# Optimization experiments

Measured on AMD Instinct MI355X. Metric: run time of the kernel, lower is better.

The kernel has to match this reference:

```python
import jax, jax.numpy as jnp
import numpy as np

B = 4096

def conv2d(x, w, b):
    # x: [B,C,H,W], w: [O,I,kh,kw]
    y = jax.lax.conv_general_dilated(x, w, (1, 1), 'VALID',
                                     dimension_numbers=('NCHW', 'OIHW', 'NCHW'))
    return y + b[None, :, None, None]

def maxpool2(x):
    return jax.lax.reduce_window(x, -jnp.inf, jax.lax.max,
                                 (1, 1, 2, 2), (1, 1, 2, 2), 'VALID')

def mdlstm(x, Wx, Whl, Whu, b, H, W, hid):
    # x: [B, C_in, H*W]; 2D LSTM scan over the HxW grid.
    Bn = x.shape[0]
    # Precompute input contribution for all cells: [H, W, B, 5*hid]
    xg = (jnp.einsum('bcn,gc->nbg', x, Wx) + b).reshape(H, W, Bn, 5 * hid)

    def row_step(carry, xg_row):
        h_up_row, c_up_row = carry  # [W, B, hid] from previous row

        def col_step(cc, inp):
            h_left, c_left = cc
            g_ij, h_up, c_up = inp
            g = g_ij + h_left @ Whl.T + h_up @ Whu.T
            i, f1, f2, o, gg = jnp.split(g, 5, axis=-1)
            c = (jax.nn.sigmoid(f1) * c_left + jax.nn.sigmoid(f2) * c_up
                 + jax.nn.sigmoid(i) * jnp.tanh(gg))
            h = jax.nn.sigmoid(o) * jnp.tanh(c)
            return (h, c), (h, c)

        z = jnp.zeros((Bn, hid), x.dtype)
        _, (h_row, c_row) = jax.lax.scan(col_step, (z, z),
                                         (xg_row, h_up_row, c_up_row))
        return (h_row, c_row), h_row

    z_row = jnp.zeros((W, Bn, hid), x.dtype)
    _, hs = jax.lax.scan(row_step, (z_row, z_row), xg)  # [H, W, B, hid]
    return hs.transpose(2, 3, 0, 1).reshape(Bn, hid, H * W)


def setup_inputs() -> dict:
    key = jax.random.key(0)
    ks = jax.random.split(key, 20)
    s = 0.1
    d = {
        'x':       jax.random.normal(ks[0], (B, 784), jnp.float32),
        'conv1_w': jax.random.normal(ks[1], (10, 1, 5, 5), jnp.float32) * s,
        'conv1_b': jnp.zeros((10,), jnp.float32),
        'm1_Wx':   jax.random.normal(ks[2], (5 * 20, 10), jnp.float32) * s,
        'm1_Whl':  jax.random.normal(ks[3], (5 * 20, 20), jnp.float32) * s,
        'm1_Whu':  jax.random.normal(ks[4], (5 * 20, 20), jnp.float32) * s,
        'm1_b':    jnp.zeros((5 * 20,), jnp.float32),
        'conv2_w': jax.random.normal(ks[5], (30, 20, 5, 5), jnp.float32) * s,
        'conv2_b': jnp.zeros((30,), jnp.float32),
        'm2_Wx':   jax.random.normal(ks[6], (5 * 40, 30), jnp.float32) * s,
        'm2_Whl':  jax.random.normal(ks[7], (5 * 40, 40), jnp.float32) * s,
        'm2_Whu':  jax.random.normal(ks[8], (5 * 40, 40), jnp.float32) * s,
        'm2_b':    jnp.zeros((5 * 40,), jnp.float32),
        'fc1_w':   jax.random.normal(ks[9], (100, 640), jnp.float32) * s,
        'fc1_b':   jnp.zeros((100,), jnp.float32),
        'fc2_w':   jax.random.normal(ks[10], (10, 100), jnp.float32) * s,
        'fc2_b':   jnp.zeros((10,), jnp.float32),
    }
    return d


def reference(x, conv1_w, conv1_b, m1_Wx, m1_Whl, m1_Whu, m1_b,
              conv2_w, conv2_b, m2_Wx, m2_Whl, m2_Whu, m2_b,
              fc1_w, fc1_b, fc2_w, fc2_b):
    h = x.reshape(-1, 1, 28, 28)
    h = jnp.tanh(maxpool2(conv2d(h, conv1_w, conv1_b)))        # [B,10,12,12]
    h = h.reshape(-1, 10, 12 * 12)
    h = mdlstm(h, m1_Wx, m1_Whl, m1_Whu, m1_b, 12, 12, 20)     # [B,20,144]
    h = h.reshape(-1, 20, 12, 12)
    h = jnp.tanh(maxpool2(conv2d(h, conv2_w, conv2_b)))        # [B,30,4,4]
    h = h.reshape(-1, 30, 4 * 4)
    h = mdlstm(h, m2_Wx, m2_Whl, m2_Whu, m2_b, 4, 4, 40)       # [B,40,16]
    h = h.reshape(-1, 4 * 4 * 40)
    h = jnp.tanh(h @ fc1_w.T + fc1_b)
    h = h @ fc2_w.T + fc2_b
    return jax.nn.softmax(h, axis=1)
```

## Files before the change

### kernel.cpp

```cpp
#include <hip/hip_runtime.h>
#include <hip/hip_bf16.h>

typedef __attribute__((ext_vector_type(8))) short sh8;
typedef __attribute__((ext_vector_type(8))) _Float16 h8;
typedef __attribute__((ext_vector_type(4))) float f4;
typedef unsigned short ushort_t;
typedef unsigned int uint_t;

__device__ __forceinline__ float fast_rcp(float x) {
    return __builtin_amdgcn_rcpf(x);
}
__device__ __forceinline__ float sigmoidf_(float x) {
    return fast_rcp(1.f + __expf(-x));
}
__device__ __forceinline__ float tanhf_fast(float x) {
    float ax = fabsf(x);
    float e  = __expf(-2.f * ax);
    float t  = (1.f - e) * fast_rcp(1.f + e);
    return copysignf(t, x);
}

__device__ __forceinline__ ushort_t f2h(float x) {
    union { _Float16 f; ushort_t u; } cv;
    cv.f = (_Float16)x;
    return cv.u;
}
__device__ __forceinline__ float h2f(ushort_t u) {
    union { _Float16 f; ushort_t u; } cv;
    cv.u = u;
    return (float)cv.f;
}
__device__ __forceinline__ int swzk(int k, int b) {
    return ((((k >> 3) ^ (b & 7)) << 3) | (k & 7));
}

__global__ __launch_bounds__(256) void conv1_pool_tanh(
    const float* __restrict__ x, const float* __restrict__ w,
    const float* __restrict__ bias, ushort_t* __restrict__ out)
{
    __shared__ float sw[250];
    __shared__ float sb[10];
    int t = threadIdx.x;
    if (t < 250) sw[t] = w[t];
    if (t < 10)  sb[t] = bias[t];
    __syncthreads();

    int gp  = blockIdx.x * 256 + t;
    int b   = gp / 144;
    int pix = gp % 144;
    int py = pix / 12, px = pix % 12;

    const float* img = x + (long)b * 784 + (2 * py) * 28 + 2 * px;
    float r[6][6];
#pragma unroll
    for (int ry = 0; ry < 6; ++ry)
#pragma unroll
        for (int rx = 0; rx < 6; ++rx)
            r[ry][rx] = img[ry * 28 + rx];

    ushort_t* ob = out + ((long)b * 144 + pix) * 10;
    for (int oc = 0; oc < 10; ++oc) {
        float a0 = 0.f, a1 = 0.f, a2 = 0.f, a3 = 0.f;
#pragma unroll
        for (int ky = 0; ky < 5; ++ky)
#pragma unroll
            for (int kx = 0; kx < 5; ++kx) {
                float wv = sw[oc * 25 + ky * 5 + kx];
                a0 += wv * r[ky][kx];
                a1 += wv * r[ky][kx + 1];
                a2 += wv * r[ky + 1][kx];
                a3 += wv * r[ky + 1][kx + 1];
            }
        float m = fmaxf(fmaxf(a0, a1), fmaxf(a2, a3)) + sb[oc];
        ob[oc] = f2h(tanhf_fast(m));
    }
}

template<int H, int HID, int CIN, int KV, int NK, int NWM, int CSPL, int TPW, int NB>
__global__ __launch_bounds__(NWM * CSPL * 64) void mdlstm_f16(
    const ushort_t* __restrict__ x, const short* __restrict__ wfm,
    const float* __restrict__ bias, ushort_t* __restrict__ out)
{
    constexpr int N    = H * H;
    constexpr int NT   = NWM * CSPL * 64;
    constexpr int HL0  = CIN, HU0 = CIN + HID;
    constexpr int SVS  = KV;
    constexpr int GS   = 5 * HID;
    constexpr int XTOT = H * NB * CIN;
    constexpr int XMAX = (XTOT + NT - 1) / NT;
    constexpr int EPT  = NB * HID;
    constexpr int CPB  = NT / EPT;
    static_assert(NWM * TPW * 16 >= 5 * HID, "tiles cover gate rows");
    static_assert(KV >= CIN + 2 * HID, "K covers V");
    static_assert(CPB >= 1, "epilogue coverage");

    __shared__ ushort_t sV[H][16][SVS];
    __shared__ float    sG[H][NB][GS];
    __shared__ float    sC[2][H][NB][HID];

    const int tid  = threadIdx.x;
    const int lane = tid & 63;
    const int wid  = tid >> 6;
    const int mth  = wid % NWM;
    const int cs   = wid / NWM;
    const int lr   = lane & 15;
    const int lg   = lane >> 4;
    const long bB  = (long)blockIdx.x * NB;

    h8 Af[TPW][NK];
    {
        const h8* wv = (const h8*)wfm;
#pragma unroll
        for (int tt = 0; tt < TPW; ++tt)
#pragma unroll
            for (int ks = 0; ks < NK; ++ks)
                Af[tt][ks] = wv[((mth * TPW + tt) * NK + ks) * 64 + lane];
    }

    f4 biasF[TPW];
#pragma unroll
    for (int tt = 0; tt < TPW; ++tt)
#pragma unroll
        for (int q = 0; q < 4; ++q) {
            int rr = (mth * TPW + tt) * 16 + lg * 4 + q;
            biasF[tt][q] = (rr < 5 * HID) ? bias[rr] : 0.f;
        }

    for (int idx = tid; idx < H * 16 * SVS; idx += NT) (&sV[0][0][0])[idx] = 0;
    __syncthreads();
    for (int idx = tid; idx < NB * CIN; idx += NT) {
        int b = idx / CIN, c = idx % CIN;
        sV[0][b][swzk(c, b)] = x[(bB + b) * (long)(N * CIN) + c];
    }
    __syncthreads();

    const bool ep_act = tid < CPB * EPT;
    const int  ep_ci0 = tid / EPT;
    const int  ep_b   = (tid % EPT) / HID;
    const int  ep_j   = tid % HID;
    const int  svl    = swzk(HL0 + ep_j, ep_b);
    const int  svu    = swzk(HU0 + ep_j, ep_b);
    ushort_t* outb = out + (bB + ep_b) * (long)(N * HID) + ep_j;

    int  xq_ci[XMAX], xq_b[XMAX], xq_off[XMAX];
    long xq_gb[XMAX];
    bool xq_ok[XMAX];
#pragma unroll
    for (int q = 0; q < XMAX; ++q) {
        int idx = tid + q * NT;
        xq_ok[q] = (idx < XTOT);
        int ci = 0, b = 0, c = 0;
        if (xq_ok[q]) { ci = idx / (NB * CIN); int rem = idx % (NB * CIN);
                        b = rem / CIN; c = rem % CIN; }
        xq_ci[q]  = ci; xq_b[q] = b;
        xq_off[q] = swzk(c, b);
        xq_gb[q]  = (bB + b) * (long)(N * CIN) + c;
    }

    for (int d = 0; d < 2 * H - 1; ++d) {
        const int i0  = (d > H - 1) ? d - (H - 1) : 0;
        const int i1  = (d < H - 1) ? d : H - 1;
        const int nc  = i1 - i0 + 1;
        const int i0n = (d + 1 > H - 1) ? d + 1 - (H - 1) : 0;
        const int i1n = (d + 1 < H - 1) ? d + 1 : H - 1;
        const int ncn = (d + 1 < 2 * H - 1) ? (i1n - i0n + 1) : 0;
        const int par = d & 1;

        for (int ci = cs; ci < nc; ci += CSPL) {
            h8 Bh[NK];
#pragma unroll
            for (int ks = 0; ks < NK; ++ks) {
                const int bo = (((ks * 4 + lg) ^ (lr & 7)) << 3);
                Bh[ks] = *(const h8*)&sV[ci][lr][bo];
            }
            f4 acc[TPW];
#pragma unroll
            for (int tt = 0; tt < TPW; ++tt) {
                acc[tt] = __builtin_amdgcn_mfma_f32_16x16x32_f16(
                              Af[tt][0], Bh[0], biasF[tt], 0, 0, 0);
#pragma unroll
                for (int ks = 1; ks < NK; ++ks)
                    acc[tt] = __builtin_amdgcn_mfma_f32_16x16x32_f16(
                                  Af[tt][ks], Bh[ks], acc[tt], 0, 0, 0);
            }
#pragma unroll
            for (int tt = 0; tt < TPW; ++tt) {
                int row4 = (mth * TPW + tt) * 16 + lg * 4;
                if (lr < NB && row4 + 4 <= 5 * HID)
                    *(f4*)&sG[ci][lr][row4] = acc[tt];
            }
        }

        ushort_t xval[XMAX];
#pragma unroll
        for (int q = 0; q < XMAX; ++q)
            if (xq_ok[q] && xq_ci[q] < ncn) {
                int ii = i0n + xq_ci[q];
                xval[q] = x[xq_gb[q] + (long)(ii * H + (d + 1 - ii)) * CIN];
            }
        __syncthreads();

        if (ep_act) {
            for (int ci = ep_ci0; ci < nc; ci += CPB) {
                const int i = i0 + ci, jc = d - i;
                const float* gp = &sG[ci][ep_b][ep_j];
                float g0 = gp[0],       g1 = gp[HID],     g2 = gp[2 * HID];
                float g3 = gp[3 * HID], g4 = gp[4 * HID];
                float c_left = (jc > 0) ? sC[par][i][ep_b][ep_j] : 0.f;
                float c_up   = (i  > 0) ? sC[par][i - 1][ep_b][ep_j] : 0.f;
                float cc = sigmoidf_(g1) * c_left + sigmoidf_(g2) * c_up
                         + sigmoidf_(g0) * tanhf_fast(g4);
                float hh = sigmoidf_(g3) * tanhf_fast(cc);
                sC[par ^ 1][i][ep_b][ep_j] = cc;
                ushort_t hv = f2h(hh);
                if (jc + 1 < H) sV[i - i0n][ep_b][svl]     = hv;
                if (i + 1 < H)  sV[i + 1 - i0n][ep_b][svu] = hv;
                outb[(i * H + jc) * HID] = hv;
            }
        }
#pragma unroll
        for (int q = 0; q < XMAX; ++q)
            if (xq_ok[q] && xq_ci[q] < ncn)
                sV[xq_ci[q]][xq_b[q]][xq_off[q]] = xval[q];
        __syncthreads();
    }
}

__global__ __launch_bounds__(256) void prep_frags(
    const float* __restrict__ wt,  short* __restrict__ wf,
    const float* __restrict__ w1,  short* __restrict__ wf1,
    const float* __restrict__ m1Wx, const float* __restrict__ m1Wl,
    const float* __restrict__ m1Wu, short* __restrict__ wfm1,
    const float* __restrict__ m2Wx, const float* __restrict__ m2Wl,
    const float* __restrict__ m2Wu, short* __restrict__ wfm2)
{
    int gid = blockIdx.x * 256 + threadIdx.x;
    if (gid < 25600) {
        int id = gid;
        int e    = id & 7;
        int lane = (id >> 3) & 63;
        int m    = (id >> 9) & 1;
        int tt   = id >> 10;
        int tx = tt / 5, ty = tt % 5;
        int c = lane & 15, kg = lane >> 4;
        int oc = m * 16 + c, ic = kg * 8 + e;
        float wv = (oc < 30 && ic < 20)
                 ? wt[((oc * 20 + ic) * 5 + ty) * 5 + tx] : 0.f;
        ushort_t wh = f2h(wv);
        ushort_t wl = f2h(wv - h2f(wh));
        wf[(((tt * 2 + m) * 2 + 0) * 64 + lane) * 8 + e] = (short)wh;
        wf[(((tt * 2 + m) * 2 + 1) * 64 + lane) * 8 + e] = (short)wl;
    } else if (gid < 25600 + 143360) {
        int id = gid - 25600;
        int e    = id & 7;
        int r    = id >> 3;
        int lane = r & 63;  r >>= 6;
        int h    = r & 1;   r >>= 1;
        int ks   = r % 20;
        int m    = r / 20;
        int o  = m * 16 + (lane & 15);
        int kp = ks * 32 + (lane >> 4) * 8 + e;
        int pix = kp / 40, hid = kp % 40;
        float wv = (o < 100) ? w1[o * 640 + hid * 16 + pix] : 0.f;
        ushort_t wh = f2h(wv);
        ushort_t v  = h ? f2h(wv - h2f(wh)) : wh;
        wf1[id] = (short)v;
    } else if (gid < 25600 + 143360 + 7168) {
        int id = gid - (25600 + 143360);
        int e    = id & 7;
        int lane = (id >> 3) & 63;
        int r    = id >> 9;
        int ks   = r & 1;
        int tt   = r >> 1;
        int rg = tt * 16 + (lane & 15);
        int k  = ks * 32 + (lane >> 4) * 8 + e;
        float wv = 0.f;
        if (rg < 100) {
            if (k < 10)       wv = m1Wx[rg * 10 + k];
            else if (k < 30)  wv = m1Wl[rg * 20 + (k - 10)];
            else if (k < 50)  wv = m1Wu[rg * 20 + (k - 30)];
        }
        wfm1[id] = (short)f2h(wv);
    } else if (gid < 25600 + 143360 + 7168 + 30720) {
        int id = gid - (25600 + 143360 + 7168);
        int e    = id & 7;
        int lane = (id >> 3) & 63;
        int r    = id >> 9;
        int ks   = r & 3;
        int q    = r >> 2;
        int tt   = q % 5;
        int mth  = q / 5;
        int rg = (mth * 5 + tt) * 16 + (lane & 15);
        int k  = ks * 32 + (lane >> 4) * 8 + e;
        float wv = 0.f;
        if (rg < 200) {
            if (k < 30)        wv = m2Wx[rg * 30 + k];
            else if (k < 70)   wv = m2Wl[rg * 40 + (k - 30)];
            else if (k < 110)  wv = m2Wu[rg * 40 + (k - 70)];
        }
        wfm2[id] = (short)f2h(wv);
    }
}

__global__ __launch_bounds__(320, 2) void conv2_mfma(
    const ushort_t* __restrict__ in, const short* __restrict__ wf,
    const float* __restrict__ bias, ushort_t* __restrict__ out)
{
    constexpr int NIMG = 16;
    __shared__ ushort_t sImg[2][144][40];
    __shared__ float    sPart[5][2][4][16][20];
    __shared__ float    sB[30];

    const int tid  = threadIdx.x;
    const int lane = tid & 63;
    const int wid  = tid >> 6;
    const int c    = lane & 15;
    const int kg   = lane >> 4;
    const long b0  = (long)blockIdx.x * NIMG;

    const h8* wfv = (const h8*)wf;
    h8 Awh[5][2], Awl[5][2];
#pragma unroll
    for (int ty = 0; ty < 5; ++ty)
#pragma unroll
        for (int m = 0; m < 2; ++m) {
            int base = (((wid * 5 + ty) * 2 + m) * 2) * 64 + lane;
            Awh[ty][m] = wfv[base];
            Awl[ty][m] = wfv[base + 64];
        }

    for (int idx = tid; idx < 2 * 144 * 20; idx += 320) {
        int bb = idx / (144 * 20);
        int r  = idx % (144 * 20);
        sImg[bb][r / 20][20 + r % 20] = 0;
    }
    if (tid < 30) sB[tid] = bias[tid];

    {
        const ushort_t* p = in + b0 * 2880;
        uint2 u0 = *(const uint2*)(p + 4 * tid);
        uint2 u1 = *(const uint2*)(p + 4 * (tid + 320));
        uint2 u2 = {0, 0};
        if (tid < 80) u2 = *(const uint2*)(p + 4 * (tid + 640));
        {
            int g = 4 * tid;          *(uint2*)&sImg[0][g / 20][g % 20] = u0;
            g = 4 * (tid + 320);      *(uint2*)&sImg[0][g / 20][g % 20] = u1;
            if (tid < 80) { g = 4 * (tid + 640);
                            *(uint2*)&sImg[0][g / 20][g % 20] = u2; }
        }
    }
    __syncthreads();

    const int y0 = c >> 3, x = c & 7;
    for (int img = 0; img < NIMG; ++img) {
        const int cb = img & 1;
        uint2 u0, u1, u2;
        const bool have = (img + 1 < NIMG);
        if (have) {
            const ushort_t* p = in + (b0 + img + 1) * 2880;
            u0 = *(const uint2*)(p + 4 * tid);
            u1 = *(const uint2*)(p + 4 * (tid + 320));
            if (tid < 80) u2 = *(const uint2*)(p + 4 * (tid + 640));
        }
#pragma unroll
        for (int p4 = 0; p4 < 4; ++p4) {
            const int pos = (2 * p4 + y0) * 12 + x + wid;
            const ushort_t* bh = &sImg[cb][pos][kg * 8];
            f4 aH0 = {0.f,0.f,0.f,0.f}, aL0 = {0.f,0.f,0.f,0.f};
            f4 aH1 = {0.f,0.f,0.f,0.f}, aL1 = {0.f,0.f,0.f,0.f};
#pragma unroll
            for (int ks = 0; ks < 5; ++ks) {
                h8 Bh = *(const h8*)(bh + ks * 12 * 40);
                aH0 = __builtin_amdgcn_mfma_f32_16x16x32_f16(Awh[ks][0], Bh, aH0, 0, 0, 0);
                aL0 = __builtin_amdgcn_mfma_f32_16x16x32_f16(Awl[ks][0], Bh, aL0, 0, 0, 0);
                aH1 = __builtin_amdgcn_mfma_f32_16x16x32_f16(Awh[ks][1], Bh, aH1, 0, 0, 0);
                aL1 = __builtin_amdgcn_mfma_f32_16x16x32_f16(Awl[ks][1], Bh, aL1, 0, 0, 0);
            }
            f4 c0 = aH0 + aL0;
            f4 c1 = aH1 + aL1;
            *(f4*)&sPart[wid][0][p4][c][kg * 4] = c0;
            *(f4*)&sPart[wid][1][p4][c][kg * 4] = c1;
        }
        if (have) {
            int g = 4 * tid;          *(uint2*)&sImg[cb ^ 1][g / 20][g % 20] = u0;
            g = 4 * (tid + 320);      *(uint2*)&sImg[cb ^ 1][g / 20][g % 20] = u1;
            if (tid < 80) { g = 4 * (tid + 640);
                            *(uint2*)&sImg[cb ^ 1][g / 20][g % 20] = u2; }
        }
        __syncthreads();
        for (int idx = tid; idx < 480; idx += 320) {
            int pix = idx / 30, oc = idx % 30;
            int m = oc >> 4, r = oc & 15;
            int py = pix >> 2, px = pix & 3;
            float vmax = -1e30f;
#pragma unroll
            for (int dy = 0; dy < 2; ++dy)
#pragma unroll
                for (int dx = 0; dx < 2; ++dx) {
                    int n = (2 * py + dy) * 8 + 2 * px + dx;
                    float s = 0.f;
#pragma unroll
                    for (int w = 0; w < 5; ++w)
                        s += sPart[w][m][n >> 4][n & 15][r];
                    vmax = fmaxf(vmax, s);
                }
            out[(b0 + img) * 480 + idx] = f2h(tanhf_fast(vmax + sB[oc]));
        }
        __syncthreads();
    }
}

__global__ __launch_bounds__(448) void fc_fused(
    const ushort_t* __restrict__ in, const short* __restrict__ wf1,
    const float* __restrict__ b1, const float* __restrict__ w2,
    const float* __restrict__ b2, float* __restrict__ out)
{
    constexpr int XS = 648;
    __shared__ ushort_t sX[16][XS];
    __shared__ float    sG[16][116];
    __shared__ float    sF[16][101];
    __shared__ float    sW2[1000];
    __shared__ float    sB2[10];
    __shared__ float    sL[16][12];

    const int tid  = threadIdx.x;
    const int lane = tid & 63;
    const int wid  = tid >> 6;
    const int lr   = lane & 15;
    const int lg   = lane >> 4;
    const long b0  = (long)blockIdx.x * 16;

    for (int idx = tid; idx < 2560; idx += 448) {
        int flat = idx * 4;
        int row = flat / 640, col = flat % 640;
        *(uint2*)&sX[row][col] =
            *(const uint2*)(in + (b0 + row) * 640 + col);
    }
    for (int idx = tid; idx < 1000; idx += 448) sW2[idx] = w2[idx];
    if (tid < 10) sB2[tid] = b2[tid];

    f4 biasF;
#pragma unroll
    for (int q = 0; q < 4; ++q) {
        int rr = wid * 16 + lg * 4 + q;
        biasF[q] = (rr < 100) ? b1[rr] : 0.f;
    }
    __syncthreads();

    {
        const h8* wfv = (const h8*)wf1;
        f4 hh = biasF, ll = {0.f, 0.f, 0.f, 0.f};
#pragma unroll
        for (int ks = 0; ks < 20; ++ks) {
            int base = ((wid * 20 + ks) * 2) * 64 + lane;
            h8 Awh = wfv[base];
            h8 Awl = wfv[base + 64];
            h8 Bh  = *(const h8*)&sX[lr][ks * 32 + lg * 8];
            hh = __builtin_amdgcn_mfma_f32_16x16x32_f16(Awh, Bh, hh, 0, 0, 0);
            ll = __builtin_amdgcn_mfma_f32_16x16x32_f16(Awl, Bh, ll, 0, 0, 0);
        }
        f4 acc = hh + ll;
        *(f4*)&sG[lr][wid * 16 + lg * 4] = acc;
    }
    __syncthreads();

    for (int idx = tid; idx < 1600; idx += 448) {
        int bb = idx / 100, o = idx % 100;
        sF[bb][o] = tanhf_fast(sG[bb][o]);
    }
    __syncthreads();

    if (tid < 160) {
        int o2 = tid >> 4, bb = tid & 15;
        const float* wr = &sW2[o2 * 100];
        float acc = sB2[o2];
        for (int k = 0; k < 100; ++k) acc += sF[bb][k] * wr[k];
        sL[bb][o2] = acc;
    }
    __syncthreads();

    if (tid < 16) {
        float lg10[10];
#pragma unroll
        for (int o = 0; o < 10; ++o) lg10[o] = sL[tid][o];
        float m = lg10[0];
#pragma unroll
        for (int o = 1; o < 10; ++o) m = fmaxf(m, lg10[o]);
        float s = 0.f;
#pragma unroll
        for (int o = 0; o < 10; ++o) { lg10[o] = __expf(lg10[o] - m); s += lg10[o]; }
        float inv = fast_rcp(s);
        float* ob = out + (b0 + tid) * 10;
#pragma unroll
        for (int o = 0; o < 10; ++o) ob[o] = lg10[o] * inv;
    }
}

extern "C" void kernel_launch(void* const* d_in, const int* in_sizes, int n_in,
                              void* d_out, int out_size, void* d_ws, size_t ws_size,
                              hipStream_t stream)
{
    const float* x    = (const float*)d_in[0];
    const float* c1w  = (const float*)d_in[1];
    const float* c1b  = (const float*)d_in[2];
    const float* m1Wx = (const float*)d_in[3];
    const float* m1Wl = (const float*)d_in[4];
    const float* m1Wu = (const float*)d_in[5];
    const float* m1b  = (const float*)d_in[6];
    const float* c2w  = (const float*)d_in[7];
    const float* c2b  = (const float*)d_in[8];
    const float* m2Wx = (const float*)d_in[9];
    const float* m2Wl = (const float*)d_in[10];
    const float* m2Wu = (const float*)d_in[11];
    const float* m2b  = (const float*)d_in[12];
    const float* f1w  = (const float*)d_in[13];
    const float* f1b  = (const float*)d_in[14];
    const float* f2w  = (const float*)d_in[15];
    const float* f2b  = (const float*)d_in[16];
    float* outp = (float*)d_out;

    char* ws = (char*)d_ws;
    ushort_t* a1 = (ushort_t*)ws;
    ushort_t* h1 = (ushort_t*)(ws + 23592960);
    ushort_t* a2 = a1;
    ushort_t* h2 = h1;
    short* wfrag  = (short*)(ws + 50331648);
    short* wfrag1 = (short*)(ws + 51380224);
    short* wfm1   = (short*)(ws + 52428800);
    short* wfm2   = (short*)(ws + 53477376);

    prep_frags<<<808, 256, 0, stream>>>(c2w, wfrag, f1w, wfrag1,
                                        m1Wx, m1Wl, m1Wu, wfm1,
                                        m2Wx, m2Wl, m2Wu, wfm2);
    conv1_pool_tanh<<<2304, 256, 0, stream>>>(x, c1w, c1b, a1);
    mdlstm_f16<12, 20, 10, 64, 2, 1, 12, 7, 16><<<256, 768, 0, stream>>>(
        a1, wfm1, m1b, h1);
    conv2_mfma<<<256, 320, 0, stream>>>(h1, wfrag, c2b, a2);
    mdlstm_f16<4, 40, 30, 128, 4, 3, 4, 5, 16><<<256, 768, 0, stream>>>(
        a2, wfm2, m2b, h2);
    fc_fused<<<256, 448, 0, stream>>>(h2, wfrag1, f1b, f2w, f2b, outp);
}
```

Baseline: 149.6 us.

## Replace first MDLSTM kernel with row-per-wave register-resident wavefront kernel

Adds a new MDLSTM kernel for the first layer in which each wave owns one grid row and walks the anti-diagonal wavefront. Weight fragments, bias and the cell state are held in registers, and the next cell's input is prefetched from global memory during the current cell's work. Gate rows for i/f1/f2/o are interleaved in the prepared weight fragments so that each lane's four MFMA accumulator outputs are the four gates of one unit, which leaves only the g-gate going through shared memory. This is meant to cut shared-memory traffic and per-step synchronization on the serial recurrence. The cost is higher register pressure, plus idle waves during the ramp-up and ramp-down of the diagonal sweep.

```diff
diff --git a/kernel.cpp b/kernel.cpp
--- a/kernel.cpp
+++ b/kernel.cpp
@@ -73,6 +73,167 @@
             }
         float m = fmaxf(fmaxf(a0, a1), fmaxf(a2, a3)) + sb[oc];
         ob[oc] = f2h(tanhf_fast(m));
+    }
+}
+
+template<int H, int HID, int CIN, int KV, int NK>
+__global__ __launch_bounds__(H * 64, 3) void mdlstm_rowreg(
+    const ushort_t* __restrict__ x, const short* __restrict__ wfm,
+    const float* __restrict__ bias, ushort_t* __restrict__ out)
+{
+    constexpr int N   = H * H;
+    constexpr int NT  = H * 64;
+    constexpr int NB  = 16;
+    constexpr int HL0 = CIN, HU0 = CIN + HID;
+    constexpr int T03 = (4 * HID) / 16;
+    constexpr int G4T = (HID + 15) / 16;
+    constexpr int TT  = T03 + G4T;
+    constexpr int UPT = HID / 4;
+    constexpr int XLD = (NB * CIN + 63) / 64;
+    static_assert((4 * HID) % 16 == 0, "gate rows align");
+    static_assert(HID % 4 == 0, "units per lg");
+    static_assert(NK * 32 == KV, "K chain covers KV");
+    static_assert(KV >= CIN + 2 * HID, "V fits");
+    static_assert(UPT * 64 == NB * HID, "store pass exact");
+
+    __shared__ ushort_t sV[2][H][NB][KV];
+    __shared__ float    sCup[2][H][NB][HID];
+    __shared__ float    sG4[H][NB][HID];
+    __shared__ ushort_t sHout[H][NB][HID];
+
+    const int tid  = threadIdx.x;
+    const int lane = tid & 63;
+    const int w    = tid >> 6;
+    const int lr   = lane & 15;
+    const int lg   = lane >> 4;
+    const long bB  = (long)blockIdx.x * NB;
+
+    h8 Af[TT][NK];
+    {
+        const h8* wv = (const h8*)wfm;
+#pragma unroll
+        for (int t = 0; t < TT; ++t)
+#pragma unroll
+            for (int ks = 0; ks < NK; ++ks)
+                Af[t][ks] = wv[(t * NK + ks) * 64 + lane];
+    }
+    f4 biasF[TT];
+#pragma unroll
+    for (int t = 0; t < TT; ++t)
+#pragma unroll
+        for (int q = 0; q < 4; ++q) {
+            int r = t * 16 + lg * 4 + q;
+            float bv = 0.f;
+            if (r < 4 * HID)      bv = bias[(r & 3) * HID + (r >> 2)];
+            else if (r < 5 * HID) bv = bias[r];
+            biasF[t][q] = bv;
+        }
+
+    for (int idx = tid; idx < 2 * H * NB * KV; idx += NT)
+        (&sV[0][0][0][0])[idx] = 0;
+    __syncthreads();
+    for (int idx = tid; idx < NB * CIN; idx += NT) {
+        int b = idx / CIN, c = idx % CIN;
+        sV[0][0][b][swzk(c, b)] = x[(bB + b) * (long)(N * CIN) + c];
+    }
+    __syncthreads();
+
+    int  xb2[XLD], xoff[XLD];
+    long xgb[XLD];
+    bool xok[XLD];
+#pragma unroll
+    for (int q = 0; q < XLD; ++q) {
+        int idx = q * 64 + lane;
+        xok[q] = idx < NB * CIN;
+        int b2 = 0, c2 = 0;
+        if (xok[q]) { b2 = idx / CIN; c2 = idx % CIN; }
+        xb2[q]  = b2;
+        xoff[q] = swzk(c2, b2);
+        xgb[q]  = (bB + b2) * (long)(N * CIN) + c2;
+    }
+    int svl[UPT], svu[UPT];
+#pragma unroll
+    for (int t = 0; t < UPT; ++t) {
+        int j = t * 4 + lg;
+        svl[t] = swzk(HL0 + j, lr);
+        svu[t] = swzk(HU0 + j, lr);
+    }
+    float creg[UPT];
+#pragma unroll
+    for (int u = 0; u < UPT; ++u) creg[u] = 0.f;
+
+    for (int d = 0; d < 2 * H - 1; ++d) {
+        const int par = d & 1;
+        const int jc  = d - w;
+        const int jn  = jc + 1;
+        const bool act  = (unsigned)jc < (unsigned)H;
+        const bool actn = (unsigned)jn < (unsigned)H;
+
+        ushort_t xr[XLD];
+        if (actn) {
+            const int co = (w * H + jn) * CIN;
+#pragma unroll
+            for (int q = 0; q < XLD; ++q)
+                if (xok[q]) xr[q] = x[xgb[q] + co];
+        }
+
+        if (act) {
+            h8 Bh[NK];
+#pragma unroll
+            for (int ks = 0; ks < NK; ++ks) {
+                const int bo = (((ks * 4 + lg) ^ (lr & 7)) << 3);
+                Bh[ks] = *(const h8*)&sV[par][w][lr][bo];
+            }
+            f4 acc[TT];
+#pragma unroll
+            for (int t = 0; t < TT; ++t) {
+                acc[t] = __builtin_amdgcn_mfma_f32_16x16x32_f16(
+                             Af[t][0], Bh[0], biasF[t], 0, 0, 0);
+#pragma unroll
+                for (int ks = 1; ks < NK; ++ks)
+                    acc[t] = __builtin_amdgcn_mfma_f32_16x16x32_f16(
+                                 Af[t][ks], Bh[ks], acc[t], 0, 0, 0);
+            }
+#pragma unroll
+            for (int g = 0; g < G4T; ++g)
+#pragma unroll
+                for (int q = 0; q < 4; ++q) {
+                    int u = g * 16 + lg * 4 + q;
+                    if (u < HID) sG4[w][lr][u] = acc[T03 + g][q];
+                }
+            const int cellOff = (w * H + jc) * HID;
+#pragma unroll
+            for (int t = 0; t < UPT; ++t) {
+                const int j = t * 4 + lg;
+                float g4 = sG4[w][lr][j];
+                float g0 = acc[t][0], g1 = acc[t][1];
+                float g2 = acc[t][2], g3 = acc[t][3];
+                float c_left = (jc > 0) ? creg[t] : 0.f;
+                float c_up   = (w > 0) ? sCup[par][w - 1][lr][j] : 0.f;
+                float cc = sigmoidf_(g1) * c_left + sigmoidf_(g2) * c_up
+                         + sigmoidf_(g0) * tanhf_fast(g4);
+                float hh = sigmoidf_(g3) * tanhf_fast(cc);
+                creg[t] = cc;
+                sCup[par ^ 1][w][lr][j] = cc;
+                ushort_t hv = f2h(hh);
+                if (jn < H)    sV[par ^ 1][w][lr][svl[t]]     = hv;
+                if (w + 1 < H) sV[par ^ 1][w + 1][lr][svu[t]] = hv;
+                sHout[w][lr][j] = hv;
+            }
+#pragma unroll
+            for (int q = 0; q < UPT; ++q) {
+                int f = q * 64 + lane;
+                int b2 = f / HID, j2 = f % HID;
+                out[(bB + b2) * (long)(N * HID) + cellOff + j2] =
+                    sHout[w][b2][j2];
+            }
+        }
+        if (actn) {
+#pragma unroll
+            for (int q = 0; q < XLD; ++q)
+                if (xok[q]) sV[par ^ 1][w][xb2[q]][xoff[q]] = xr[q];
+        }
+        __syncthreads();
     }
 }
 
@@ -271,14 +432,17 @@
         int lane = (id >> 3) & 63;
         int r    = id >> 9;
         int ks   = r & 1;
-        int tt   = r >> 1;
-        int rg = tt * 16 + (lane & 15);
+        int t    = r >> 1;
+        int rg = t * 16 + (lane & 15);
         int k  = ks * 32 + (lane >> 4) * 8 + e;
+        int orig = -1;
+        if (rg < 80)       orig = (rg & 3) * 20 + (rg >> 2);
+        else if (rg < 100) orig = rg;
         float wv = 0.f;
-        if (rg < 100) {
-            if (k < 10)       wv = m1Wx[rg * 10 + k];
-            else if (k < 30)  wv = m1Wl[rg * 20 + (k - 10)];
-            else if (k < 50)  wv = m1Wu[rg * 20 + (k - 30)];
+        if (orig >= 0) {
+            if (k < 10)       wv = m1Wx[orig * 10 + k];
+            else if (k < 30)  wv = m1Wl[orig * 20 + (k - 10)];
+            else if (k < 50)  wv = m1Wu[orig * 20 + (k - 30)];
         }
         wfm1[id] = (short)f2h(wv);
     } else if (gid < 25600 + 143360 + 7168 + 30720) {
@@ -533,7 +697,7 @@
                                         m1Wx, m1Wl, m1Wu, wfm1,
                                         m2Wx, m2Wl, m2Wu, wfm2);
     conv1_pool_tanh<<<2304, 256, 0, stream>>>(x, c1w, c1b, a1);
-    mdlstm_f16<12, 20, 10, 64, 2, 1, 12, 7, 16><<<256, 768, 0, stream>>>(
+    mdlstm_rowreg<12, 20, 10, 64, 2><<<256, 768, 0, stream>>>(
         a1, wfm1, m1b, h1);
     conv2_mfma<<<256, 320, 0, stream>>>(h1, wfrag, c2b, a2);
     mdlstm_f16<4, 40, 30, 128, 4, 3, 4, 5, 16><<<256, 768, 0, stream>>>(
```

Result: slower. 223.4 us (+49.3%).

## Fuse second MDLSTM layer with FC head into one kernel

Applied to the files above, without the earlier changes.

Merges the 4x4 MDLSTM kernel and the fully connected/softmax kernel into a single kernel. The MDLSTM hidden outputs stay in shared memory as fp16 and feed the FC1 MFMA directly, and the gate scratch buffer is reused for the FC intermediates. This removes one kernel launch and a global write and read of the [B,640] hidden tensor. In exchange the block holds more shared memory, and 7 of 12 waves sit idle during the FC phase.

```diff
diff --git a/kernel.cpp b/kernel.cpp
--- a/kernel.cpp
+++ b/kernel.cpp
@@ -223,6 +223,220 @@
             if (xq_ok[q] && xq_ci[q] < ncn)
                 sV[xq_ci[q]][xq_b[q]][xq_off[q]] = xval[q];
         __syncthreads();
+    }
+}
+
+__global__ __launch_bounds__(768) void m2fc_fused(
+    const ushort_t* __restrict__ x, const short* __restrict__ wfm,
+    const float* __restrict__ bias, const short* __restrict__ wf1,
+    const float* __restrict__ b1, const float* __restrict__ w2,
+    const float* __restrict__ b2, float* __restrict__ out)
+{
+    constexpr int H = 4, HID = 40, CIN = 30, KV = 128, NK = 4;
+    constexpr int NWM = 3, CSPL = 4, TPW = 5, NB = 16;
+    constexpr int N    = 16;
+    constexpr int NT   = 768;
+    constexpr int HL0  = CIN, HU0 = CIN + HID;
+    constexpr int SVS  = KV;
+    constexpr int GS   = 5 * HID;
+    constexpr int XTOT = H * NB * CIN;
+    constexpr int XMAX = 3;
+    constexpr int EPT  = NB * HID;
+    constexpr int XS   = 648;
+
+    __shared__ ushort_t sV[H][16][SVS];
+    __shared__ float    sG[H][NB][GS];
+    __shared__ float    sC[2][H][NB][HID];
+    __shared__ ushort_t sH2[16][XS];
+
+    const int tid  = threadIdx.x;
+    const int lane = tid & 63;
+    const int wid  = tid >> 6;
+    const int mth  = wid % NWM;
+    const int cs   = wid / NWM;
+    const int lr   = lane & 15;
+    const int lg   = lane >> 4;
+    const long bB  = (long)blockIdx.x * NB;
+
+    h8 Af[TPW][NK];
+    {
+        const h8* wv = (const h8*)wfm;
+#pragma unroll
+        for (int tt = 0; tt < TPW; ++tt)
+#pragma unroll
+            for (int ks = 0; ks < NK; ++ks)
+                Af[tt][ks] = wv[((mth * TPW + tt) * NK + ks) * 64 + lane];
+    }
+    f4 biasF[TPW];
+#pragma unroll
+    for (int tt = 0; tt < TPW; ++tt)
+#pragma unroll
+        for (int q = 0; q < 4; ++q) {
+            int rr = (mth * TPW + tt) * 16 + lg * 4 + q;
+            biasF[tt][q] = (rr < 5 * HID) ? bias[rr] : 0.f;
+        }
+
+    for (int idx = tid; idx < H * 16 * SVS; idx += NT) (&sV[0][0][0])[idx] = 0;
+    __syncthreads();
+    for (int idx = tid; idx < NB * CIN; idx += NT) {
+        int b = idx / CIN, c = idx % CIN;
+        sV[0][b][swzk(c, b)] = x[(bB + b) * (long)(N * CIN) + c];
+    }
+    __syncthreads();
+
+    const bool ep_act = tid < EPT;
+    const int  ep_b   = (tid % EPT) / HID;
+    const int  ep_j   = tid % HID;
+    const int  svl    = swzk(HL0 + ep_j, ep_b);
+    const int  svu    = swzk(HU0 + ep_j, ep_b);
+
+    int  xq_ci[XMAX], xq_b[XMAX], xq_off[XMAX];
+    long xq_gb[XMAX];
+    bool xq_ok[XMAX];
+#pragma unroll
+    for (int q = 0; q < XMAX; ++q) {
+        int idx = tid + q * NT;
+        xq_ok[q] = (idx < XTOT);
+        int ci = 0, b = 0, c = 0;
+        if (xq_ok[q]) { ci = idx / (NB * CIN); int rem = idx % (NB * CIN);
+                        b = rem / CIN; c = rem % CIN; }
+        xq_ci[q]  = ci; xq_b[q] = b;
+        xq_off[q] = swzk(c, b);
+        xq_gb[q]  = (bB + b) * (long)(N * CIN) + c;
+    }
+
+    for (int d = 0; d < 2 * H - 1; ++d) {
+        const int i0  = (d > H - 1) ? d - (H - 1) : 0;
+        const int i1  = (d < H - 1) ? d : H - 1;
+        const int nc  = i1 - i0 + 1;
+        const int i0n = (d + 1 > H - 1) ? d + 1 - (H - 1) : 0;
+        const int i1n = (d + 1 < H - 1) ? d + 1 : H - 1;
+        const int ncn = (d + 1 < 2 * H - 1) ? (i1n - i0n + 1) : 0;
+        const int par = d & 1;
+
+        for (int ci = cs; ci < nc; ci += CSPL) {
+            h8 Bh[NK];
+#pragma unroll
+            for (int ks = 0; ks < NK; ++ks) {
+                const int bo = (((ks * 4 + lg) ^ (lr & 7)) << 3);
+                Bh[ks] = *(const h8*)&sV[ci][lr][bo];
+            }
+            f4 acc[TPW];
+#pragma unroll
+            for (int tt = 0; tt < TPW; ++tt) {
+                acc[tt] = __builtin_amdgcn_mfma_f32_16x16x32_f16(
+                              Af[tt][0], Bh[0], biasF[tt], 0, 0, 0);
+#pragma unroll
+                for (int ks = 1; ks < NK; ++ks)
+                    acc[tt] = __builtin_amdgcn_mfma_f32_16x16x32_f16(
+                                  Af[tt][ks], Bh[ks], acc[tt], 0, 0, 0);
+            }
+#pragma unroll
+            for (int tt = 0; tt < TPW; ++tt) {
+                int row4 = (mth * TPW + tt) * 16 + lg * 4;
+                if (lr < NB && row4 + 4 <= 5 * HID)
+                    *(f4*)&sG[ci][lr][row4] = acc[tt];
+            }
+        }
+
+        ushort_t xval[XMAX];
+#pragma unroll
+        for (int q = 0; q < XMAX; ++q)
+            if (xq_ok[q] && xq_ci[q] < ncn) {
+                int ii = i0n + xq_ci[q];
+                xval[q] = x[xq_gb[q] + (long)(ii * H + (d + 1 - ii)) * CIN];
+            }
+        __syncthreads();
+
+        if (ep_act) {
+            for (int ci = 0; ci < nc; ++ci) {
+                const int i = i0 + ci, jc = d - i;
+                const float* gp = &sG[ci][ep_b][ep_j];
+                float g0 = gp[0],       g1 = gp[HID],     g2 = gp[2 * HID];
+                float g3 = gp[3 * HID], g4 = gp[4 * HID];
+                float c_left = (jc > 0) ? sC[par][i][ep_b][ep_j] : 0.f;
+                float c_up   = (i  > 0) ? sC[par][i - 1][ep_b][ep_j] : 0.f;
+                float cc = sigmoidf_(g1) * c_left + sigmoidf_(g2) * c_up
+                         + sigmoidf_(g0) * tanhf_fast(g4);
+                float hh = sigmoidf_(g3) * tanhf_fast(cc);
+                sC[par ^ 1][i][ep_b][ep_j] = cc;
+                ushort_t hv = f2h(hh);
+                if (jc + 1 < H) sV[i - i0n][ep_b][svl]     = hv;
+                if (i + 1 < H)  sV[i + 1 - i0n][ep_b][svu] = hv;
+                sH2[ep_b][(i * H + jc) * HID + ep_j] = hv;
+            }
+        }
+#pragma unroll
+        for (int q = 0; q < XMAX; ++q)
+            if (xq_ok[q] && xq_ci[q] < ncn)
+                sV[xq_ci[q]][xq_b[q]][xq_off[q]] = xval[q];
+        __syncthreads();
+    }
+
+    float* scratch = &sG[0][0][0];
+    float* fcG = scratch;
+    float* sF  = scratch + 1856;
+    float* sW2 = scratch + 3472;
+    float* sB2 = scratch + 4472;
+    float* sL  = scratch + 4482;
+
+    for (int idx = tid; idx < 1000; idx += NT) sW2[idx] = w2[idx];
+    if (tid < 10) sB2[tid] = b2[tid];
+
+    f4 bF;
+#pragma unroll
+    for (int q = 0; q < 4; ++q) {
+        int rr = wid * 16 + lg * 4 + q;
+        bF[q] = (rr < 100) ? b1[rr] : 0.f;
+    }
+    __syncthreads();
+
+    if (wid < 7) {
+        const h8* wfv = (const h8*)wf1;
+        f4 hh = bF, ll = {0.f, 0.f, 0.f, 0.f};
+#pragma unroll
+        for (int ks = 0; ks < 20; ++ks) {
+            int base = ((wid * 20 + ks) * 2) * 64 + lane;
+            h8 Awh = wfv[base];
+            h8 Awl = wfv[base + 64];
+            h8 Bh  = *(const h8*)&sH2[lr][ks * 32 + lg * 8];
+            hh = __builtin_amdgcn_mfma_f32_16x16x32_f16(Awh, Bh, hh, 0, 0, 0);
+            ll = __builtin_amdgcn_mfma_f32_16x16x32_f16(Awl, Bh, ll, 0, 0, 0);
+        }
+        f4 acc = hh + ll;
+        *(f4*)&fcG[lr * 116 + wid * 16 + lg * 4] = acc;
+    }
+    __syncthreads();
+
+    for (int idx = tid; idx < 1600; idx += NT) {
+        int bb = idx / 100, o = idx % 100;
+        sF[bb * 101 + o] = tanhf_fast(fcG[bb * 116 + o]);
+    }
+    __syncthreads();
+
+    if (tid < 160) {
+        int o2 = tid >> 4, bb = tid & 15;
+        const float* wr = &sW2[o2 * 100];
+        float acc = sB2[o2];
+        for (int k = 0; k < 100; ++k) acc += sF[bb * 101 + k] * wr[k];
+        sL[bb * 12 + o2] = acc;
+    }
+    __syncthreads();
+
+    if (tid < 16) {
+        float lg10[10];
+#pragma unroll
+        for (int o = 0; o < 10; ++o) lg10[o] = sL[tid * 12 + o];
+        float m = lg10[0];
+#pragma unroll
+        for (int o = 1; o < 10; ++o) m = fmaxf(m, lg10[o]);
+        float s = 0.f;
+#pragma unroll
+        for (int o = 0; o < 10; ++o) { lg10[o] = __expf(lg10[o] - m); s += lg10[o]; }
+        float inv = fast_rcp(s);
+        float* ob = out + (bB + tid) * 10;
+#pragma unroll
+        for (int o = 0; o < 10; ++o) ob[o] = lg10[o] * inv;
     }
 }
 
@@ -410,92 +624,6 @@
     }
 }
 
-__global__ __launch_bounds__(448) void fc_fused(
-    const ushort_t* __restrict__ in, const short* __restrict__ wf1,
-    const float* __restrict__ b1, const float* __restrict__ w2,
-    const float* __restrict__ b2, float* __restrict__ out)
-{
-    constexpr int XS = 648;
-    __shared__ ushort_t sX[16][XS];
-    __shared__ float    sG[16][116];
-    __shared__ float    sF[16][101];
-    __shared__ float    sW2[1000];
-    __shared__ float    sB2[10];
-    __shared__ float    sL[16][12];
-
-    const int tid  = threadIdx.x;
-    const int lane = tid & 63;
-    const int wid  = tid >> 6;
-    const int lr   = lane & 15;
-    const int lg   = lane >> 4;
-    const long b0  = (long)blockIdx.x * 16;
-
-    for (int idx = tid; idx < 2560; idx += 448) {
-        int flat = idx * 4;
-        int row = flat / 640, col = flat % 640;
-        *(uint2*)&sX[row][col] =
-            *(const uint2*)(in + (b0 + row) * 640 + col);
-    }
-    for (int idx = tid; idx < 1000; idx += 448) sW2[idx] = w2[idx];
-    if (tid < 10) sB2[tid] = b2[tid];
-
-    f4 biasF;
-#pragma unroll
-    for (int q = 0; q < 4; ++q) {
-        int rr = wid * 16 + lg * 4 + q;
-        biasF[q] = (rr < 100) ? b1[rr] : 0.f;
-    }
-    __syncthreads();
-
-    {
-        const h8* wfv = (const h8*)wf1;
-        f4 hh = biasF, ll = {0.f, 0.f, 0.f, 0.f};
-#pragma unroll
-        for (int ks = 0; ks < 20; ++ks) {
-            int base = ((wid * 20 + ks) * 2) * 64 + lane;
-            h8 Awh = wfv[base];
-            h8 Awl = wfv[base + 64];
-            h8 Bh  = *(const h8*)&sX[lr][ks * 32 + lg * 8];
-            hh = __builtin_amdgcn_mfma_f32_16x16x32_f16(Awh, Bh, hh, 0, 0, 0);
-            ll = __builtin_amdgcn_mfma_f32_16x16x32_f16(Awl, Bh, ll, 0, 0, 0);
-        }
-        f4 acc = hh + ll;
-        *(f4*)&sG[lr][wid * 16 + lg * 4] = acc;
-    }
-    __syncthreads();
-
-    for (int idx = tid; idx < 1600; idx += 448) {
-        int bb = idx / 100, o = idx % 100;
-        sF[bb][o] = tanhf_fast(sG[bb][o]);
-    }
-    __syncthreads();
-
-    if (tid < 160) {
-        int o2 = tid >> 4, bb = tid & 15;
-        const float* wr = &sW2[o2 * 100];
-        float acc = sB2[o2];
-        for (int k = 0; k < 100; ++k) acc += sF[bb][k] * wr[k];
-        sL[bb][o2] = acc;
-    }
-    __syncthreads();
-
-    if (tid < 16) {
-        float lg10[10];
-#pragma unroll
-        for (int o = 0; o < 10; ++o) lg10[o] = sL[tid][o];
-        float m = lg10[0];
-#pragma unroll
-        for (int o = 1; o < 10; ++o) m = fmaxf(m, lg10[o]);
-        float s = 0.f;
-#pragma unroll
-        for (int o = 0; o < 10; ++o) { lg10[o] = __expf(lg10[o] - m); s += lg10[o]; }
-        float inv = fast_rcp(s);
-        float* ob = out + (b0 + tid) * 10;
-#pragma unroll
-        for (int o = 0; o < 10; ++o) ob[o] = lg10[o] * inv;
-    }
-}
-
 extern "C" void kernel_launch(void* const* d_in, const int* in_sizes, int n_in,
                               void* d_out, int out_size, void* d_ws, size_t ws_size,
                               hipStream_t stream)
@@ -523,7 +651,6 @@
     ushort_t* a1 = (ushort_t*)ws;
     ushort_t* h1 = (ushort_t*)(ws + 23592960);
     ushort_t* a2 = a1;
-    ushort_t* h2 = h1;
     short* wfrag  = (short*)(ws + 50331648);
     short* wfrag1 = (short*)(ws + 51380224);
     short* wfm1   = (short*)(ws + 52428800);
@@ -536,7 +663,6 @@
     mdlstm_f16<12, 20, 10, 64, 2, 1, 12, 7, 16><<<256, 768, 0, stream>>>(
         a1, wfm1, m1b, h1);
     conv2_mfma<<<256, 320, 0, stream>>>(h1, wfrag, c2b, a2);
-    mdlstm_f16<4, 40, 30, 128, 4, 3, 4, 5, 16><<<256, 768, 0, stream>>>(
-        a2, wfm2, m2b, h2);
-    fc_fused<<<256, 448, 0, stream>>>(h2, wfrag1, f1b, f2w, f2b, outp);
-}
+    m2fc_fused<<<256, 768, 0, stream>>>(a2, wfm2, m2b, wfrag1,
+                                        f1b, f2w, f2b, outp);
+}
```

Measured after the change: 144.6 us (median of 2 runs). -3.3%, faster.
